# Kernel optimization log

Measured on AMD Instinct MI355X. Metric: run time of the kernel, lower is better.

Reference implementation:

```python
import jax, jax.numpy as jnp
import numpy as np

N, H, W, K, F, D = 16, 512, 512, 1, 9976, 12


def setup_inputs() -> dict:
    key = jax.random.key(0)
    k1, k2, k3 = jax.random.split(key, 3)
    # pix_to_face: global (batch-flattened) face index per pixel, -1 = background
    pix_to_face = jax.random.randint(k1, (N, H, W, K), -1, N * F, dtype=jnp.int64)
    # barycentric weights, normalized to sum to 1 per pixel
    b = jax.random.uniform(k2, (N, H, W, K, 3), dtype=jnp.float32) + 1e-3
    bary_coords = b / jnp.sum(b, axis=-1, keepdims=True)
    # per-face per-corner attributes: uv(3)+transformed_normal(3)+position(3)+normal(3)
    attributes = jax.random.normal(k3, (N, F, 3, D), dtype=jnp.float32)
    return {"pix_to_face": pix_to_face, "bary_coords": bary_coords, "attributes": attributes}


def reference(pix_to_face, bary_coords, attributes):
    # Faithful translation of the shared interpolation tail of
    # Pytorch3dRasterizer/StandardRasterizer.forward.
    n, h, w, k = pix_to_face.shape
    d = attributes.shape[-1]
    mask = pix_to_face < 0                              # [N,H,W,K] background pixels
    idx = jnp.where(mask, 0, pix_to_face)               # clamp -1 -> 0 (torch: pix_to_face[mask]=0)
    flat_attr = attributes.reshape(-1, 3, d)            # [N*F, 3, D]
    pixel_face_vals = flat_attr[idx]                    # gather -> [N,H,W,K,3,D]
    # barycentric-weighted sum over the 3 triangle corners
    pixel_vals = jnp.einsum('nhwkv,nhwkvd->nhwkd', bary_coords, pixel_face_vals)
    pixel_vals = jnp.where(mask[..., None], jnp.asarray(0.0, pixel_vals.dtype), pixel_vals)
    pixel_vals = jnp.transpose(pixel_vals[:, :, :, 0, :], (0, 3, 1, 2))  # [N,D,H,W]
    vismask = (pix_to_face[:, :, :, 0] > -1).astype(pixel_vals.dtype)[:, None]  # [N,1,H,W]
    return jnp.concatenate([pixel_vals, vismask], axis=1)  # [N,D+1,H,W]
```

## Files before the change

### kernel.cpp

```cpp
#include <hip/hip_runtime.h>

#define PN 16
#define PH 512
#define PW 512
#define PF 9976
#define PD 12

__global__ __launch_bounds__(256) void interp_face_attrs_kernel(
    const int*   __restrict__ pix_to_face,
    const float* __restrict__ bary,
    const float* __restrict__ attr,
    float*       __restrict__ out)
{
    const int HW     = PH * PW;
    const int total4 = PN * HW / 4;
    int tid = blockIdx.x * blockDim.x + threadIdx.x;
    if (tid >= total4) return;

    const int base = tid * 4;
    const int n    = base / HW;
    const int hw   = base - n * HW;

    const int4 p4 = *reinterpret_cast<const int4*>(pix_to_face + base);

    const float4* bq = reinterpret_cast<const float4*>(bary + (size_t)base * 3);
    const float4 bA = bq[0];
    const float4 bB = bq[1];
    const float4 bC = bq[2];

    const int   pi[4] = { p4.x, p4.y, p4.z, p4.w };
    const float bw[4][3] = {
        { bA.x, bA.y, bA.z },
        { bA.w, bB.x, bB.y },
        { bB.z, bB.w, bC.x },
        { bC.y, bC.z, bC.w },
    };

    float v[PD + 1][4];

    #pragma unroll
    for (int i = 0; i < 4; ++i) {
        const int p = pi[i];
        if (p < 0) {
            #pragma unroll
            for (int d = 0; d <= PD; ++d) v[d][i] = 0.0f;
        } else {
            const float4* a4 = reinterpret_cast<const float4*>(attr + (size_t)p * (3 * PD));
            float a[36];
            #pragma unroll
            for (int j = 0; j < 9; ++j) {
                float4 t = a4[j];
                a[4 * j + 0] = t.x;
                a[4 * j + 1] = t.y;
                a[4 * j + 2] = t.z;
                a[4 * j + 3] = t.w;
            }
            const float b0 = bw[i][0], b1 = bw[i][1], b2 = bw[i][2];
            #pragma unroll
            for (int d = 0; d < PD; ++d) {
                v[d][i] = b0 * a[d] + b1 * a[PD + d] + b2 * a[2 * PD + d];
            }
            v[PD][i] = 1.0f;
        }
    }

    float* o = out + (size_t)n * (PD + 1) * HW + hw;
    #pragma unroll
    for (int d = 0; d <= PD; ++d) {
        float4 s = { v[d][0], v[d][1], v[d][2], v[d][3] };
        *reinterpret_cast<float4*>(o + (size_t)d * HW) = s;
    }
}

extern "C" void kernel_launch(void* const* d_in, const int* in_sizes, int n_in,
                              void* d_out, int out_size, void* d_ws, size_t ws_size,
                              hipStream_t stream) {
    const int*   pix_to_face = (const int*)d_in[0];
    const float* bary        = (const float*)d_in[1];
    const float* attr        = (const float*)d_in[2];
    float*       out         = (float*)d_out;

    const int total4 = PN * PH * PW / 4;
    const int block  = 256;
    const int grid   = (total4 + block - 1) / block;

    interp_face_attrs_kernel<<<grid, block, 0, stream>>>(pix_to_face, bary, attr, out);
}
```

Baseline: 395.3 us.

## Convert face attributes to padded fp16 table and use nontemporal streaming loads/stores

Measured after the change: 349.1 us. -11.7%, faster.

```diff
diff --git a/kernel.cpp b/kernel.cpp
--- a/kernel.cpp
+++ b/kernel.cpp
@@ -1,16 +1,50 @@
 #include <hip/hip_runtime.h>
+#include <hip/hip_fp16.h>
 
 #define PN 16
 #define PH 512
 #define PW 512
 #define PF 9976
 #define PD 12
+#define NFACES (PN * PF)
+#define REC 40
 
-__global__ __launch_bounds__(256) void interp_face_attrs_kernel(
-    const int*   __restrict__ pix_to_face,
-    const float* __restrict__ bary,
+typedef int          v4i __attribute__((ext_vector_type(4)));
+typedef float        v4f __attribute__((ext_vector_type(4)));
+typedef unsigned int v4u __attribute__((ext_vector_type(4)));
+
+__global__ __launch_bounds__(256) void convert_attr_kernel(
     const float* __restrict__ attr,
-    float*       __restrict__ out)
+    __half*      __restrict__ tab)
+{
+    int f = blockIdx.x * blockDim.x + threadIdx.x;
+    if (f >= NFACES) return;
+
+    const v4f* src = reinterpret_cast<const v4f*>(attr + (size_t)f * 36);
+    float a[36];
+    #pragma unroll
+    for (int j = 0; j < 9; ++j) {
+        v4f t = src[j];
+        a[4 * j + 0] = t.x; a[4 * j + 1] = t.y;
+        a[4 * j + 2] = t.z; a[4 * j + 3] = t.w;
+    }
+
+    union { __half h[REC]; v4u q[REC / 8]; } w;
+    #pragma unroll
+    for (int j = 0; j < 36; ++j) w.h[j] = __float2half(a[j]);
+    #pragma unroll
+    for (int j = 36; j < REC; ++j) w.h[j] = __half(0.0f);
+
+    v4u* dst = reinterpret_cast<v4u*>(tab + (size_t)f * REC);
+    #pragma unroll
+    for (int j = 0; j < REC / 8; ++j) dst[j] = w.q[j];
+}
+
+__global__ __launch_bounds__(256) void interp_fp16_kernel(
+    const int*    __restrict__ pix_to_face,
+    const float*  __restrict__ bary,
+    const __half* __restrict__ tab,
+    float*        __restrict__ out)
 {
     const int HW     = PH * PW;
     const int total4 = PN * HW / 4;
@@ -21,14 +55,15 @@
     const int n    = base / HW;
     const int hw   = base - n * HW;
 
-    const int4 p4 = *reinterpret_cast<const int4*>(pix_to_face + base);
+    const v4i p4 = __builtin_nontemporal_load(
+        reinterpret_cast<const v4i*>(pix_to_face + base));
 
-    const float4* bq = reinterpret_cast<const float4*>(bary + (size_t)base * 3);
-    const float4 bA = bq[0];
-    const float4 bB = bq[1];
-    const float4 bC = bq[2];
+    const v4f* bq = reinterpret_cast<const v4f*>(bary + (size_t)base * 3);
+    const v4f bA = __builtin_nontemporal_load(bq + 0);
+    const v4f bB = __builtin_nontemporal_load(bq + 1);
+    const v4f bC = __builtin_nontemporal_load(bq + 2);
 
-    const int   pi[4] = { p4.x, p4.y, p4.z, p4.w };
+    const int   pi[4]    = { p4.x, p4.y, p4.z, p4.w };
     const float bw[4][3] = {
         { bA.x, bA.y, bA.z },
         { bA.w, bB.x, bB.y },
@@ -45,20 +80,18 @@
             #pragma unroll
             for (int d = 0; d <= PD; ++d) v[d][i] = 0.0f;
         } else {
-            const float4* a4 = reinterpret_cast<const float4*>(attr + (size_t)p * (3 * PD));
-            float a[36];
+            const __half* af = tab + (size_t)p * REC;
+            union { v4u q[5]; __half h[40]; } u;
+            const v4u* g = reinterpret_cast<const v4u*>(af);
             #pragma unroll
-            for (int j = 0; j < 9; ++j) {
-                float4 t = a4[j];
-                a[4 * j + 0] = t.x;
-                a[4 * j + 1] = t.y;
-                a[4 * j + 2] = t.z;
-                a[4 * j + 3] = t.w;
-            }
+            for (int j = 0; j < 5; ++j) u.q[j] = g[j];
+
             const float b0 = bw[i][0], b1 = bw[i][1], b2 = bw[i][2];
             #pragma unroll
             for (int d = 0; d < PD; ++d) {
-                v[d][i] = b0 * a[d] + b1 * a[PD + d] + b2 * a[2 * PD + d];
+                v[d][i] = b0 * __half2float(u.h[d])
+                        + b1 * __half2float(u.h[PD + d])
+                        + b2 * __half2float(u.h[2 * PD + d]);
             }
             v[PD][i] = 1.0f;
         }
@@ -67,8 +100,70 @@
     float* o = out + (size_t)n * (PD + 1) * HW + hw;
     #pragma unroll
     for (int d = 0; d <= PD; ++d) {
-        float4 s = { v[d][0], v[d][1], v[d][2], v[d][3] };
-        *reinterpret_cast<float4*>(o + (size_t)d * HW) = s;
+        v4f s = { v[d][0], v[d][1], v[d][2], v[d][3] };
+        __builtin_nontemporal_store(s, reinterpret_cast<v4f*>(o + (size_t)d * HW));
+    }
+}
+
+__global__ __launch_bounds__(256) void interp_f32_kernel(
+    const int*   __restrict__ pix_to_face,
+    const float* __restrict__ bary,
+    const float* __restrict__ attr,
+    float*       __restrict__ out)
+{
+    const int HW     = PH * PW;
+    const int total4 = PN * HW / 4;
+    int tid = blockIdx.x * blockDim.x + threadIdx.x;
+    if (tid >= total4) return;
+
+    const int base = tid * 4;
+    const int n    = base / HW;
+    const int hw   = base - n * HW;
+
+    const v4i p4 = __builtin_nontemporal_load(
+        reinterpret_cast<const v4i*>(pix_to_face + base));
+    const v4f* bq = reinterpret_cast<const v4f*>(bary + (size_t)base * 3);
+    const v4f bA = __builtin_nontemporal_load(bq + 0);
+    const v4f bB = __builtin_nontemporal_load(bq + 1);
+    const v4f bC = __builtin_nontemporal_load(bq + 2);
+
+    const int   pi[4]    = { p4.x, p4.y, p4.z, p4.w };
+    const float bw[4][3] = {
+        { bA.x, bA.y, bA.z },
+        { bA.w, bB.x, bB.y },
+        { bB.z, bB.w, bC.x },
+        { bC.y, bC.z, bC.w },
+    };
+
+    float v[PD + 1][4];
+    #pragma unroll
+    for (int i = 0; i < 4; ++i) {
+        const int p = pi[i];
+        if (p < 0) {
+            #pragma unroll
+            for (int d = 0; d <= PD; ++d) v[d][i] = 0.0f;
+        } else {
+            const v4f* a4 = reinterpret_cast<const v4f*>(attr + (size_t)p * 36);
+            float a[36];
+            #pragma unroll
+            for (int j = 0; j < 9; ++j) {
+                v4f t = a4[j];
+                a[4 * j + 0] = t.x; a[4 * j + 1] = t.y;
+                a[4 * j + 2] = t.z; a[4 * j + 3] = t.w;
+            }
+            const float b0 = bw[i][0], b1 = bw[i][1], b2 = bw[i][2];
+            #pragma unroll
+            for (int d = 0; d < PD; ++d)
+                v[d][i] = b0 * a[d] + b1 * a[PD + d] + b2 * a[2 * PD + d];
+            v[PD][i] = 1.0f;
+        }
+    }
+
+    float* o = out + (size_t)n * (PD + 1) * HW + hw;
+    #pragma unroll
+    for (int d = 0; d <= PD; ++d) {
+        v4f s = { v[d][0], v[d][1], v[d][2], v[d][3] };
+        __builtin_nontemporal_store(s, reinterpret_cast<v4f*>(o + (size_t)d * HW));
     }
 }
 
@@ -84,5 +179,14 @@
     const int block  = 256;
     const int grid   = (total4 + block - 1) / block;
 
-    interp_face_attrs_kernel<<<grid, block, 0, stream>>>(pix_to_face, bary, attr, out);
+    const size_t need_ws = (size_t)NFACES * REC * sizeof(__half);
+
+    if (ws_size >= need_ws) {
+        __half* tab = (__half*)d_ws;
+        const int cgrid = (NFACES + block - 1) / block;
+        convert_attr_kernel<<<cgrid, block, 0, stream>>>(attr, tab);
+        interp_fp16_kernel<<<grid, block, 0, stream>>>(pix_to_face, bary, tab, out);
+    } else {
+        interp_f32_kernel<<<grid, block, 0, stream>>>(pix_to_face, bary, attr, out);
+    }
 }
```
